# Kernel tuning notes

Measured on AMD Instinct MI355X. Metric: run time of the kernel, lower is better.

Reference implementation:

```python
import math
import jax, jax.numpy as jnp
import numpy as np

NUM_HEADS = 32

def _alibi_slopes(n: int) -> jnp.ndarray:
    cp2 = 2 ** int(math.floor(math.log2(n)))
    base = 2.0 ** (-(2.0 ** (-(math.log2(cp2) - 3))))
    slopes = base ** np.arange(1, cp2 + 1, dtype=np.float64)
    if cp2 != n:
        extra_base = 2.0 ** (-(2.0 ** (-(math.log2(2 * cp2) - 3))))
        rem = min(cp2, n - cp2)
        slopes = np.concatenate([slopes, extra_base ** np.arange(1, 1 + 2 * rem, 2, dtype=np.float64)])
    return jnp.asarray(slopes, dtype=jnp.float32)


def setup_inputs() -> dict:
    key = jax.random.key(0)
    k1, k2, k3 = jax.random.split(key, 3)
    B, S, E, H, D = 2, 2048, 4096, NUM_HEADS, 128
    hidden_states = jax.random.normal(k1, (B, S, E), dtype=jnp.float32)
    # torch Linear y = x @ W^T; we store transposed weights [in, out]
    w_qkv = jax.random.normal(k2, (E, H * D + 2 * D), dtype=jnp.float32) * 0.02
    w_c = jax.random.normal(k3, (E, E), dtype=jnp.float32) * 0.02
    return {"hidden_states": hidden_states, "w_qkv": w_qkv, "w_c": w_c}


def reference(hidden_states, w_qkv, w_c):
    B, S, E = hidden_states.shape
    H = NUM_HEADS
    D = E // H
    scaling = D ** -0.5

    qkv = hidden_states @ w_qkv                      # [B,S,H*D+2D]
    q = qkv[..., : H * D].reshape(B, S, H, D)        # [B,S,H,D]
    k = qkv[..., H * D: H * D + D]                   # [B,S,D] single KV head (MQA)
    v = qkv[..., H * D + D:]                         # [B,S,D]

    pos = jnp.arange(S)
    slopes = _alibi_slopes(H)                        # [H]
    # ALiBi: slope * (k_pos - q_pos), <= 0 in the causal region
    bias = slopes[:, None, None] * (pos[None, None, :] - pos[None, :, None]).astype(jnp.float32)  # [H,S,S]

    scores = jnp.einsum('bqhd,bkd->bhqk', q, k) * scaling + bias[None]  # [B,H,S,S]
    causal = pos[:, None] >= pos[None, :]            # [S,S]
    scores = jnp.where(causal[None, None], scores, jnp.finfo(scores.dtype).min)
    probs = jax.nn.softmax(scores, axis=-1)
    attn = jnp.einsum('bhqk,bkd->bqhd', probs, v).reshape(B, S, E)
    return attn @ w_c
```

## Files before the change

kernel.cpp:

```cpp
#include <hip/hip_runtime.h>
#include <hip/hip_bf16.h>

typedef unsigned short u16;
typedef unsigned int u32;
typedef __attribute__((ext_vector_type(8))) short s16x8;
typedef __attribute__((ext_vector_type(4))) float f32x4;

#define MFMA_BF16(a, b, c) __builtin_amdgcn_mfma_f32_16x16x32_bf16(a, b, c, 0, 0, 0)

__device__ __forceinline__ u16 f2bf(float f) {
  union { float f; u32 u; } c; c.f = f;
  return (u16)((c.u + 0x7FFFu + ((c.u >> 16) & 1u)) >> 16);
}

__device__ __forceinline__ u32 pkbf(float a, float b) {
  float2 t; t.x = a; t.y = b;
  __hip_bfloat162 h = __float22bfloat162_rn(t);
  union { __hip_bfloat162 h; u32 u; } c; c.h = h; return c.u;
}

__device__ __forceinline__ void gll16(const void* g, void* l) {
  __builtin_amdgcn_global_load_lds((const __attribute__((address_space(1))) void*)g,
                                   (__attribute__((address_space(3))) void*)l, 16, 0, 0);
}

__device__ __forceinline__ f32x4 f4zero() { f32x4 z = {0.f, 0.f, 0.f, 0.f}; return z; }

__global__ void cvt_bf16_kernel(const float4* __restrict__ in, u16* __restrict__ out, int n4) {
  int i = blockIdx.x * 256 + threadIdx.x;
  if (i >= n4) return;
  float4 v = in[i];
  uint2 w;
  w.x = (u32)f2bf(v.x) | ((u32)f2bf(v.y) << 16);
  w.y = (u32)f2bf(v.z) | ((u32)f2bf(v.w) << 16);
  *reinterpret_cast<uint2*>(out + (size_t)i * 4) = w;
}

__global__ void transpose_cvt_kernel(const float* __restrict__ in, u16* __restrict__ out,
                                     int R, int C) {
  __shared__ float tile[32][33];
  int tx = threadIdx.x, ty = threadIdx.y;
  int r0 = blockIdx.y * 32, c0 = blockIdx.x * 32;
#pragma unroll
  for (int i = 0; i < 32; i += 8)
    tile[ty + i][tx] = in[(size_t)(r0 + ty + i) * C + c0 + tx];
  __syncthreads();
#pragma unroll
  for (int i = 0; i < 32; i += 8)
    out[(size_t)(c0 + ty + i) * R + r0 + tx] = f2bf(tile[tx][ty + i]);
}


#define BARRIER __builtin_amdgcn_s_barrier()
#define LGKM0 asm volatile("s_waitcnt lgkmcnt(0)" ::: "memory")
#define PRIO1 __builtin_amdgcn_s_setprio(1)
#define PRIO0 __builtin_amdgcn_s_setprio(0)
#define VM6 asm volatile("s_waitcnt vmcnt(6)" ::: "memory")
#define VM4 asm volatile("s_waitcnt vmcnt(4)" ::: "memory")
#define VM2 asm volatile("s_waitcnt vmcnt(2)" ::: "memory")
#define VM0 asm volatile("s_waitcnt vmcnt(0)" ::: "memory")
#define NOPSTMT do {} while (0)
#define W1EPI do { if constexpr (EPI == 1) { VM6; } else { VM2; } } while (0)

#define RD_A(dst, PR, QM) do { _Pragma("unroll")                                         \
  for (int mi2 = 0; mi2 < 4; ++mi2) {                                                    \
    dst[mi2][0] = *(const s16x8*)(smem + (PR)*32768 + (QM)*16384 + mi2*2048 + aOff0);    \
    dst[mi2][1] = *(const s16x8*)(smem + (PR)*32768 + (QM)*16384 + mi2*2048 + aOff1);    \
  } } while (0)

#define RD_B(dst, PR, QN) do { _Pragma("unroll")                                         \
  for (int ni2 = 0; ni2 < 2; ++ni2) {                                                    \
    dst[ni2][0] = *(const s16x8*)(smem + 65536 + (PR)*32768 + (QN)*16384 + ni2*2048 + bOff0); \
    dst[ni2][1] = *(const s16x8*)(smem + 65536 + (PR)*32768 + (QN)*16384 + ni2*2048 + bOff1); \
  } } while (0)

#define MFMA_Q(QM, QN, Af, Bf) do { _Pragma("unroll")                                    \
  for (int ks = 0; ks < 2; ++ks) { _Pragma("unroll")                                     \
    for (int mi2 = 0; mi2 < 4; ++mi2) { _Pragma("unroll")                                \
      for (int ni2 = 0; ni2 < 2; ++ni2)                                                  \
        acc[(QM)*4+mi2][(QN)*2+ni2] =                                                    \
            MFMA_BF16(Af[mi2][ks], Bf[ni2][ks], acc[(QM)*4+mi2][(QN)*2+ni2]);            \
  } } } while (0)

#define STAGE_PAIR(x, PW, kn) do {                                                       \
  gll16(srcA[x] + (kn), smem + (PW)*32768 + (x)*8192 + tt*16);                           \
  gll16(srcB[x] + (kn), smem + 65536 + (PW)*32768 + (x)*8192 + tt*16);                   \
} while (0)

#define TILE_BODY(PR, KB, S1, S2, S3, S4, W1, W4) do {                                   \
  s16x8 a0[4][2], a1[4][2], b0[2][2], b1[2][2];                                          \
  s16x8 bkv[2][2]; s16x8 sa[2];                                                          \
                                                                           \
  RD_A(a0, PR, 0); RD_B(b0, PR, 0);                                                      \
  if constexpr (EPI == 1) {                                                              \
    const u16* kvp = Bt + (size_t)(4096 + w * 32 + li) * K + (KB) + g * 8;               \
    bkv[0][0] = *(const s16x8*)(kvp);                                                    \
    bkv[0][1] = *(const s16x8*)(kvp + 32);                                               \
    bkv[1][0] = *(const s16x8*)(kvp + (size_t)16 * K);                                   \
    bkv[1][1] = *(const s16x8*)(kvp + (size_t)16 * K + 32);                              \
  }                                                                                      \
  S1;                                                                                    \
  BARRIER; LGKM0; PRIO1; MFMA_Q(0, 0, a0, b0); PRIO0;                                    \
  W1; BARRIER;                                                                           \
                                                                           \
  RD_B(b1, PR, 1);                                                                       \
  S2;                                                                                    \
  BARRIER; LGKM0; PRIO1; MFMA_Q(0, 1, a0, b1); PRIO0; BARRIER;                           \
                                                                           \
  RD_A(a1, PR, 1);                                                                       \
  S3;                                                                                    \
  BARRIER; LGKM0; PRIO1; MFMA_Q(1, 1, a1, b1); PRIO0; BARRIER;                           \
                                                                \
  RD_B(b0, PR, 0);                                                                       \
  if constexpr (EPI == 1) {                                                              \
    sa[0] = *(const s16x8*)(smem + (PR)*32768 + aKV);                                    \
    sa[1] = *(const s16x8*)(smem + (PR)*32768 + (aKV ^ 64));                             \
  }                                                                                      \
  S4;                                                                                    \
  BARRIER; LGKM0; PRIO1; MFMA_Q(1, 0, a1, b0);                                           \
  if constexpr (EPI == 1) { _Pragma("unroll")                                            \
    for (int ks2 = 0; ks2 < 2; ++ks2) { _Pragma("unroll")                                \
      for (int cs2 = 0; cs2 < 2; ++cs2)                                                  \
        acc_kv[cs2] = MFMA_BF16(sa[ks2], bkv[cs2][ks2], acc_kv[cs2]);                    \
  } }                                                                                    \
  PRIO0; W4; BARRIER;                                                                    \
} while (0)

#define TILE_MAIN(PR, PW, T) TILE_BODY(PR, (T)*64,                                       \
  STAGE_PAIR(0, PW, ((T)+1)*64), STAGE_PAIR(1, PW, ((T)+1)*64),                          \
  STAGE_PAIR(2, PW, ((T)+1)*64), STAGE_PAIR(3, PW, ((T)+1)*64), W1EPI, VM4)
#define TILE_LAST(PR, T) TILE_BODY(PR, (T)*64, NOPSTMT, NOPSTMT, NOPSTMT, NOPSTMT, VM0, NOPSTMT)

template<int EPI>
__global__ __launch_bounds__(512, 2)
void gemm256_kernel(const u16* __restrict__ A, const u16* __restrict__ Bt,
                    float* __restrict__ Cf, u16* __restrict__ Cq,
                    u16* __restrict__ Ck, u16* __restrict__ Cvt,
                    int N, int K) {
  __shared__ __align__(16) char smem[131072];
  const int tt = threadIdx.x;
  const int w = tt >> 6, l = tt & 63;
  const int li = l & 15, g = l >> 4;
  const int wm = w >> 2, wn = w & 3;

  const int gx = gridDim.x;
  const int nwg = gx * gridDim.y;
  int id = blockIdx.y * gx + blockIdx.x;
  id = (id & 7) * (nwg >> 3) + (id >> 3);
  const int bn = id % gx, bm = id / gx;

  f32x4 acc[8][4];
#pragma unroll
  for (int i = 0; i < 8; ++i)
#pragma unroll
    for (int j = 0; j < 4; ++j) acc[i][j] = f4zero();
  f32x4 acc_kv[2];
  acc_kv[0] = f4zero(); acc_kv[1] = f4zero();

  const int q8 = (((tt & 7) ^ ((tt >> 3) & 7)) * 8);
  const u16* srcA[4];
  const u16* srcB[4];
#pragma unroll
  for (int x = 0; x < 4; ++x) {
    const int arow = (x & 1) * 128 + (x >> 1) * 64 + (tt >> 3);
    srcA[x] = A + (size_t)(bm * 256 + arow) * K + q8;
    const int rho = x * 64 + (tt >> 3);
    const int qn_ = rho >> 7, rem = rho & 127;
    const int wn_ = rem >> 5, rr = rem & 31;
    const int brow = wn_ * 64 + qn_ * 32 + rr;
    srcB[x] = Bt + (size_t)(bn * 256 + brow) * K + q8;
  }

  const int gr0 = (g ^ (li & 7)) * 16;
  const int aOff0 = wm * 8192 + li * 128 + gr0;
  const int aOff1 = aOff0 ^ 64;
  const int bOff0 = wn * 4096 + li * 128 + gr0;
  const int bOff1 = bOff0 ^ 64;
  const int aKV = ((bn >> 2) & 1) * 16384 + (bn >> 3) * 8192 + (bn & 3) * 2048
                  + li * 128 + gr0;

#pragma unroll
  for (int x = 0; x < 4; ++x) STAGE_PAIR(x, 0, 0);
  VM0;
  BARRIER;

  for (int t2 = 0; t2 < 62; t2 += 2) {
    TILE_MAIN(0, 1, t2);
    TILE_MAIN(1, 0, t2 + 1);
  }
  TILE_MAIN(0, 1, 62);
  TILE_LAST(1, 63);

#pragma unroll
  for (int mi = 0; mi < 8; ++mi) {
#pragma unroll
    for (int ni = 0; ni < 4; ++ni) {
      const int row0 = bm * 256 + wm * 128 + mi * 16 + g * 4;
      const int col = bn * 256 + wn * 64 + ni * 16 + li;
#pragma unroll
      for (int r = 0; r < 4; ++r) {
        const int m = row0 + r;
        const float v = acc[mi][ni][r];
        if (EPI == 0) {
          Cf[(size_t)m * N + col] = v;
        } else {
          Cq[(size_t)m * 4096 + col] = f2bf(v);
        }
      }
    }
  }
  if constexpr (EPI == 1) {
#pragma unroll
    for (int cs = 0; cs < 2; ++cs) {
      const int col = 4096 + w * 32 + cs * 16 + li;
#pragma unroll
      for (int r = 0; r < 4; ++r) {
        const int m = bm * 256 + bn * 16 + g * 4 + r;
        const float v = acc_kv[cs][r];
        const int bb2 = m >> 11, s = m & 2047;
        const int kt = s >> 5;
        const size_t tb = (size_t)(bb2 * 64 + kt);
        if (col < 4224) {
          const int d = col - 4096, kr = s & 31;
          const int mk = kr >> 4, lii = kr & 15;
          const int kk = d >> 5, gg = (d >> 3) & 3, e = d & 7;
          Ck[(tb * 8 + mk * 4 + kk) * 512 + (gg * 16 + lii) * 8 + e] = f2bf(v);
        } else {
          const int d = col - 4224, kp = s & 31;
          const int mf = d >> 4, lii = d & 15;
          const int gg = kp >> 3, e = kp & 7;
          Cvt[(tb * 8 + mf) * 512 + (gg * 16 + lii) * 8 + e] = f2bf(v);
        }
      }
    }
  }
}


__device__ __forceinline__ void load_ktile(s16x8 (&dst)[8], const u16* kf, size_t tb, int l) {
#pragma unroll
  for (int f = 0; f < 8; ++f)
    dst[f] = *(const s16x8*)&kf[(tb * 8 + f) * 512 + l * 8];
}

template<bool DIAG>
__device__ __forceinline__ void attn_tile(
    int kt, const u16* kf, const u16* vf, size_t bb64, int l, int li, int g,
    s16x8 (&use)[8], s16x8 (&fill)[8], bool do_fill,
    const s16x8 (&bq)[2][4], f32x4 (&acc)[8][2],
    float (&m_)[2], float (&lp)[2], float (&bias)[2],
    float c1, const float (&cjr)[8], float bstep, u16 (*Pw)[40]) {
  const size_t tb = bb64 + kt;
  s16x8 vr[8];
#pragma unroll
  for (int f = 0; f < 8; ++f)
    vr[f] = *(const s16x8*)&vf[(tb * 8 + f) * 512 + l * 8];
  if (do_fill) load_ktile(fill, kf, tb - 1, l);

  f32x4 sc[2][2];
  sc[0][0] = f4zero(); sc[0][1] = f4zero(); sc[1][0] = f4zero(); sc[1][1] = f4zero();
#pragma unroll
  for (int kk = 0; kk < 4; ++kk)
#pragma unroll
    for (int mk = 0; mk < 2; ++mk) {
      sc[mk][0] = MFMA_BF16(use[mk * 4 + kk], bq[0][kk], sc[mk][0]);
      sc[mk][1] = MFMA_BF16(use[mk * 4 + kk], bq[1][kk], sc[mk][1]);
    }

#pragma unroll
  for (int nq = 0; nq < 2; ++nq) {
    float sv[8];
    float pm = -3e38f;
    if (DIAG) {
#pragma unroll
      for (int mk = 0; mk < 2; ++mk)
#pragma unroll
        for (int r = 0; r < 4; ++r) {
          const int kd = mk * 16 + g * 4 + r - (nq * 16 + li);
          float s = fmaf(sc[mk][nq][r], c1, bias[nq] + cjr[mk * 4 + r]);
          s = (kd <= 0) ? s : -1e30f;
          sv[mk * 4 + r] = s;
          pm = fmaxf(pm, s);
        }
      pm = fmaxf(pm, __shfl_xor(pm, 16));
      pm = fmaxf(pm, __shfl_xor(pm, 32));
      m_[nq] = pm;
    } else {
#pragma unroll
      for (int mk = 0; mk < 2; ++mk)
#pragma unroll
        for (int r = 0; r < 4; ++r) {
          float s = fmaf(sc[mk][nq][r], c1, bias[nq] + cjr[mk * 4 + r]);
          sv[mk * 4 + r] = s;
          pm = fmaxf(pm, s);
        }
      if (__any(pm > m_[nq])) {
        pm = fmaxf(pm, __shfl_xor(pm, 16));
        pm = fmaxf(pm, __shfl_xor(pm, 32));
        const float nm = fmaxf(m_[nq], pm);
        const float scale = exp2f(m_[nq] - nm);
#pragma unroll
        for (int mf = 0; mf < 8; ++mf) acc[mf][nq] *= scale;
        lp[nq] *= scale;
        m_[nq] = nm;
      }
    }
    const float mref = m_[nq];
    float e[8];
#pragma unroll
    for (int j = 0; j < 8; ++j) e[j] = exp2f(sv[j] - mref);
    lp[nq] += ((e[0] + e[1]) + (e[2] + e[3])) + ((e[4] + e[5]) + (e[6] + e[7]));
#pragma unroll
    for (int mk = 0; mk < 2; ++mk) {
      uint2 wv;
      wv.x = pkbf(e[mk * 4 + 0], e[mk * 4 + 1]);
      wv.y = pkbf(e[mk * 4 + 2], e[mk * 4 + 3]);
      *reinterpret_cast<uint2*>(&Pw[nq * 16 + li][mk * 16 + g * 4]) = wv;
    }
    bias[nq] -= bstep;
  }

  s16x8 pb0 = *(const s16x8*)&Pw[li][g * 8];
  s16x8 pb1 = *(const s16x8*)&Pw[16 + li][g * 8];
#pragma unroll
  for (int mf = 0; mf < 8; ++mf) {
    acc[mf][0] = MFMA_BF16(vr[mf], pb0, acc[mf][0]);
    acc[mf][1] = MFMA_BF16(vr[mf], pb1, acc[mf][1]);
  }
}

__device__ __forceinline__ void attn_qtile(
    int qt, int h, int b, const u16* qbuf, const u16* kf, const u16* vf,
    u16* obuf, int l, int li, int g, float c1, float sl2, u16 (*Pw)[40]) {
  const int S = 2048;
  const int q0 = qt * 32;
  const size_t bb64 = (size_t)b * 64;

  s16x8 bq[2][4];
#pragma unroll
  for (int nq = 0; nq < 2; ++nq)
#pragma unroll
    for (int kk = 0; kk < 4; ++kk)
      bq[nq][kk] = *(const s16x8*)&qbuf[(size_t)(b * S + q0 + nq * 16 + li) * 4096
                                        + h * 128 + kk * 32 + g * 8];

  f32x4 acc[8][2];
#pragma unroll
  for (int mf = 0; mf < 8; ++mf) { acc[mf][0] = f4zero(); acc[mf][1] = f4zero(); }
  float m_[2] = {-3e38f, -3e38f};
  float lp[2] = {0.f, 0.f};

  float cjr[8];
#pragma unroll
  for (int j = 0; j < 8; ++j) cjr[j] = sl2 * (float)((j >> 2) * 16 + (j & 3));
  float bias[2];
#pragma unroll
  for (int nq = 0; nq < 2; ++nq)
    bias[nq] = sl2 * (float)(g * 4 - nq * 16 - li);
  const float bstep = sl2 * 32.f;

  s16x8 kA[8], kB[8];
  load_ktile(kA, kf, bb64 + qt, l);
  attn_tile<true>(qt, kf, vf, bb64, l, li, g, kA, kB, qt >= 1,
                  bq, acc, m_, lp, bias, c1, cjr, bstep, Pw);
  int kt = qt - 1;
  while (kt >= 1) {
    attn_tile<false>(kt, kf, vf, bb64, l, li, g, kB, kA, true,
                     bq, acc, m_, lp, bias, c1, cjr, bstep, Pw);
    attn_tile<false>(kt - 1, kf, vf, bb64, l, li, g, kA, kB, kt >= 2,
                     bq, acc, m_, lp, bias, c1, cjr, bstep, Pw);
    kt -= 2;
  }
  if (kt == 0)
    attn_tile<false>(0, kf, vf, bb64, l, li, g, kB, kA, false,
                     bq, acc, m_, lp, bias, c1, cjr, bstep, Pw);

#pragma unroll
  for (int nq = 0; nq < 2; ++nq) {
    float ls = lp[nq];
    ls += __shfl_xor(ls, 16);
    ls += __shfl_xor(ls, 32);
    const float inv = 1.f / ls;
    const size_t rowbase = (size_t)(b * S + q0 + nq * 16 + li) * 4096 + h * 128;
#pragma unroll
    for (int mf = 0; mf < 8; ++mf) {
      f32x4 v = acc[mf][nq];
      uint2 wv;
      wv.x = pkbf(v[0] * inv, v[1] * inv);
      wv.y = pkbf(v[2] * inv, v[3] * inv);
      *reinterpret_cast<uint2*>(&obuf[rowbase + mf * 16 + g * 4]) = wv;
    }
  }
}

__global__ __launch_bounds__(64, 2)
void attn_kernel(const u16* __restrict__ qbuf, const u16* __restrict__ kf,
                 const u16* __restrict__ vf, u16* __restrict__ obuf) {
  const int p = blockIdx.x, h = blockIdx.y, b = blockIdx.z;
  const int l = threadIdx.x, li = l & 15, g = l >> 4;
  const float L2E = 1.4426950408889634f;
  const float slope = exp2f(-0.25f * (float)(h + 1));
  const float c1 = 0.08838834764831845f * L2E;
  const float sl2 = slope * L2E;
  __shared__ __align__(16) u16 P[32][40];
  attn_qtile(63 - p, h, b, qbuf, kf, vf, obuf, l, li, g, c1, sl2, P);
  attn_qtile(p, h, b, qbuf, kf, vf, obuf, l, li, g, c1, sl2, P);
}

extern "C" void kernel_launch(void* const* d_in, const int* in_sizes, int n_in,
                              void* d_out, int out_size, void* d_ws, size_t ws_size,
                              hipStream_t stream) {
  (void)in_sizes; (void)n_in; (void)out_size; (void)ws_size;
  const float* hidden = (const float*)d_in[0];
  const float* w_qkv = (const float*)d_in[1];
  const float* w_c = (const float*)d_in[2];
  float* out = (float*)d_out;
  char* ws = (char*)d_ws;

  u16* hid_bf = (u16*)(ws + 0);
  u16* wT     = (u16*)(ws + 33554432);
  u16* qbuf   = (u16*)(ws + 69206016);
  u16* kbuf   = (u16*)(ws + 102760448);
  u16* vtbuf  = (u16*)(ws + 103809024);

  cvt_bf16_kernel<<<16384, 256, 0, stream>>>((const float4*)hidden, hid_bf, 4194304);
  transpose_cvt_kernel<<<dim3(136, 128), dim3(32, 8), 0, stream>>>(w_qkv, wT, 4096, 4352);
  gemm256_kernel<1><<<dim3(16, 16), 512, 0, stream>>>(hid_bf, wT, nullptr, qbuf, kbuf, vtbuf,
                                                      4352, 4096);
  attn_kernel<<<dim3(32, 32, 2), 64, 0, stream>>>(qbuf, kbuf, vtbuf, hid_bf);
  transpose_cvt_kernel<<<dim3(128, 128), dim3(32, 8), 0, stream>>>(w_c, wT, 4096, 4096);
  gemm256_kernel<0><<<dim3(16, 16), 512, 0, stream>>>(hid_bf, wT, out, nullptr, nullptr, nullptr,
                                                      4096, 4096);
}
```

Baseline: 485.8 us.

## Restructure GEMM main loop into two K-half phases with register double-buffered fragments

```diff
diff --git a/kernel.cpp b/kernel.cpp
--- a/kernel.cpp
+++ b/kernel.cpp
@@ -53,83 +53,73 @@
 
 #define BARRIER __builtin_amdgcn_s_barrier()
 #define LGKM0 asm volatile("s_waitcnt lgkmcnt(0)" ::: "memory")
+#define LGKM12 asm volatile("s_waitcnt lgkmcnt(12)" ::: "memory")
 #define PRIO1 __builtin_amdgcn_s_setprio(1)
 #define PRIO0 __builtin_amdgcn_s_setprio(0)
-#define VM6 asm volatile("s_waitcnt vmcnt(6)" ::: "memory")
-#define VM4 asm volatile("s_waitcnt vmcnt(4)" ::: "memory")
-#define VM2 asm volatile("s_waitcnt vmcnt(2)" ::: "memory")
 #define VM0 asm volatile("s_waitcnt vmcnt(0)" ::: "memory")
-#define NOPSTMT do {} while (0)
-#define W1EPI do { if constexpr (EPI == 1) { VM6; } else { VM2; } } while (0)
-
-#define RD_A(dst, PR, QM) do { _Pragma("unroll")                                         \
-  for (int mi2 = 0; mi2 < 4; ++mi2) {                                                    \
-    dst[mi2][0] = *(const s16x8*)(smem + (PR)*32768 + (QM)*16384 + mi2*2048 + aOff0);    \
-    dst[mi2][1] = *(const s16x8*)(smem + (PR)*32768 + (QM)*16384 + mi2*2048 + aOff1);    \
+
+#define RD12(AA, BB, PRB, KX) do { _Pragma("unroll")                                     \
+  for (int q = 0; q < 2; ++q) { _Pragma("unroll")                                        \
+    for (int m = 0; m < 4; ++m)                                                          \
+      AA[q*4+m] = *(const s16x8*)(smem + (PRB) + q*16384 + m*2048 + (aOff0 ^ (KX))); }   \
+  _Pragma("unroll")                                                                      \
+  for (int q = 0; q < 2; ++q) { _Pragma("unroll")                                        \
+    for (int n = 0; n < 2; ++n)                                                          \
+      BB[q*2+n] = *(const s16x8*)(smem + 65536 + (PRB) + q*16384 + n*2048 + (bOff0 ^ (KX))); } \
+} while (0)
+
+#define MFMA32(AA, BB) do { _Pragma("unroll")                                            \
+  for (int q = 0; q < 2; ++q) { _Pragma("unroll")                                        \
+    for (int m = 0; m < 4; ++m) { _Pragma("unroll")                                      \
+      for (int p = 0; p < 2; ++p) { _Pragma("unroll")                                    \
+        for (int n = 0; n < 2; ++n)                                                      \
+          acc[q*4+m][p*2+n] = MFMA_BF16(AA[q*4+m], BB[p*2+n], acc[q*4+m][p*2+n]);        \
+  } } } } while (0)
+
+#define STAGE4(PWB, kn) do { _Pragma("unroll")                                           \
+  for (int x = 0; x < 4; ++x) {                                                          \
+    gll16(srcA0 + (size_t)ADROW[x] * K + (kn), smem + (PWB) + x*8192 + tt*16);           \
+    gll16(srcB[x] + (kn), smem + 65536 + (PWB) + x*8192 + tt*16);                        \
   } } while (0)
 
-#define RD_B(dst, PR, QN) do { _Pragma("unroll")                                         \
-  for (int ni2 = 0; ni2 < 2; ++ni2) {                                                    \
-    dst[ni2][0] = *(const s16x8*)(smem + 65536 + (PR)*32768 + (QN)*16384 + ni2*2048 + bOff0); \
-    dst[ni2][1] = *(const s16x8*)(smem + 65536 + (PR)*32768 + (QN)*16384 + ni2*2048 + bOff1); \
-  } } while (0)
-
-#define MFMA_Q(QM, QN, Af, Bf) do { _Pragma("unroll")                                    \
-  for (int ks = 0; ks < 2; ++ks) { _Pragma("unroll")                                     \
-    for (int mi2 = 0; mi2 < 4; ++mi2) { _Pragma("unroll")                                \
-      for (int ni2 = 0; ni2 < 2; ++ni2)                                                  \
-        acc[(QM)*4+mi2][(QN)*2+ni2] =                                                    \
-            MFMA_BF16(Af[mi2][ks], Bf[ni2][ks], acc[(QM)*4+mi2][(QN)*2+ni2]);            \
-  } } } while (0)
-
-#define STAGE_PAIR(x, PW, kn) do {                                                       \
-  gll16(srcA[x] + (kn), smem + (PW)*32768 + (x)*8192 + tt*16);                           \
-  gll16(srcB[x] + (kn), smem + 65536 + (PW)*32768 + (x)*8192 + tt*16);                   \
+#define TILE(PRB, PWB, T, LAST) do {                                                     \
+               \
+  if constexpr (EPI == 1) {                                                              \
+    const u16* kvp = Bt + (size_t)(4096 + w * 32 + li) * K + (T) * 64 + g * 8;           \
+    bkv[0] = *(const s16x8*)(kvp);                                                       \
+    bkv[1] = *(const s16x8*)(kvp + (size_t)16 * K);                                      \
+    sa = *(const s16x8*)(smem + (PRB) + aKV);                                            \
+  }                                                                                      \
+  RD12(Ab, Bb, PRB, 64);                                                                 \
+  if (!(LAST)) { STAGE4(PWB, ((T) + 1) * 64); }                                          \
+  BARRIER;                                                                               \
+  LGKM12;                                                                                \
+  PRIO1; MFMA32(Aa, Ba);                                                                 \
+  if constexpr (EPI == 1) {                                                              \
+    acc_kv[0] = MFMA_BF16(sa, bkv[0], acc_kv[0]);                                        \
+    acc_kv[1] = MFMA_BF16(sa, bkv[1], acc_kv[1]);                                        \
+  }                                                                                      \
+  PRIO0;                                                                                 \
+  VM0;                                                                                   \
+  BARRIER;                                                                               \
+            \
+  if constexpr (EPI == 1) {                                                              \
+    const u16* kvp = Bt + (size_t)(4096 + w * 32 + li) * K + (T) * 64 + g * 8;           \
+    bkv[0] = *(const s16x8*)(kvp + 32);                                                  \
+    bkv[1] = *(const s16x8*)(kvp + (size_t)16 * K + 32);                                 \
+    sa = *(const s16x8*)(smem + (PRB) + (aKV ^ 64));                                     \
+  }                                                                                      \
+  if (!(LAST)) { RD12(Aa, Ba, PWB, 0); }                                                 \
+  BARRIER;                                                                               \
+  if (LAST) { LGKM0; } else { LGKM12; }                                                  \
+  PRIO1; MFMA32(Ab, Bb);                                                                 \
+  if constexpr (EPI == 1) {                                                              \
+    acc_kv[0] = MFMA_BF16(sa, bkv[0], acc_kv[0]);                                        \
+    acc_kv[1] = MFMA_BF16(sa, bkv[1], acc_kv[1]);                                        \
+  }                                                                                      \
+  PRIO0;                                                                                 \
+  BARRIER;                                                                               \
 } while (0)
-
-#define TILE_BODY(PR, KB, S1, S2, S3, S4, W1, W4) do {                                   \
-  s16x8 a0[4][2], a1[4][2], b0[2][2], b1[2][2];                                          \
-  s16x8 bkv[2][2]; s16x8 sa[2];                                                          \
-                                                                           \
-  RD_A(a0, PR, 0); RD_B(b0, PR, 0);                                                      \
-  if constexpr (EPI == 1) {                                                              \
-    const u16* kvp = Bt + (size_t)(4096 + w * 32 + li) * K + (KB) + g * 8;               \
-    bkv[0][0] = *(const s16x8*)(kvp);                                                    \
-    bkv[0][1] = *(const s16x8*)(kvp + 32);                                               \
-    bkv[1][0] = *(const s16x8*)(kvp + (size_t)16 * K);                                   \
-    bkv[1][1] = *(const s16x8*)(kvp + (size_t)16 * K + 32);                              \
-  }                                                                                      \
-  S1;                                                                                    \
-  BARRIER; LGKM0; PRIO1; MFMA_Q(0, 0, a0, b0); PRIO0;                                    \
-  W1; BARRIER;                                                                           \
-                                                                           \
-  RD_B(b1, PR, 1);                                                                       \
-  S2;                                                                                    \
-  BARRIER; LGKM0; PRIO1; MFMA_Q(0, 1, a0, b1); PRIO0; BARRIER;                           \
-                                                                           \
-  RD_A(a1, PR, 1);                                                                       \
-  S3;                                                                                    \
-  BARRIER; LGKM0; PRIO1; MFMA_Q(1, 1, a1, b1); PRIO0; BARRIER;                           \
-                                                                \
-  RD_B(b0, PR, 0);                                                                       \
-  if constexpr (EPI == 1) {                                                              \
-    sa[0] = *(const s16x8*)(smem + (PR)*32768 + aKV);                                    \
-    sa[1] = *(const s16x8*)(smem + (PR)*32768 + (aKV ^ 64));                             \
-  }                                                                                      \
-  S4;                                                                                    \
-  BARRIER; LGKM0; PRIO1; MFMA_Q(1, 0, a1, b0);                                           \
-  if constexpr (EPI == 1) { _Pragma("unroll")                                            \
-    for (int ks2 = 0; ks2 < 2; ++ks2) { _Pragma("unroll")                                \
-      for (int cs2 = 0; cs2 < 2; ++cs2)                                                  \
-        acc_kv[cs2] = MFMA_BF16(sa[ks2], bkv[cs2][ks2], acc_kv[cs2]);                    \
-  } }                                                                                    \
-  PRIO0; W4; BARRIER;                                                                    \
-} while (0)
-
-#define TILE_MAIN(PR, PW, T) TILE_BODY(PR, (T)*64,                                       \
-  STAGE_PAIR(0, PW, ((T)+1)*64), STAGE_PAIR(1, PW, ((T)+1)*64),                          \
-  STAGE_PAIR(2, PW, ((T)+1)*64), STAGE_PAIR(3, PW, ((T)+1)*64), W1EPI, VM4)
-#define TILE_LAST(PR, T) TILE_BODY(PR, (T)*64, NOPSTMT, NOPSTMT, NOPSTMT, NOPSTMT, VM0, NOPSTMT)
 
 template<int EPI>
 __global__ __launch_bounds__(512, 2)
@@ -142,6 +132,7 @@
   const int w = tt >> 6, l = tt & 63;
   const int li = l & 15, g = l >> 4;
   const int wm = w >> 2, wn = w & 3;
+  constexpr int ADROW[4] = {0, 128, 64, 192};
 
   const int gx = gridDim.x;
   const int nwg = gx * gridDim.y;
@@ -158,12 +149,10 @@
   acc_kv[0] = f4zero(); acc_kv[1] = f4zero();
 
   const int q8 = (((tt & 7) ^ ((tt >> 3) & 7)) * 8);
-  const u16* srcA[4];
+  const u16* srcA0 = A + (size_t)(bm * 256 + (tt >> 3)) * K + q8;
   const u16* srcB[4];
 #pragma unroll
   for (int x = 0; x < 4; ++x) {
-    const int arow = (x & 1) * 128 + (x >> 1) * 64 + (tt >> 3);
-    srcA[x] = A + (size_t)(bm * 256 + arow) * K + q8;
     const int rho = x * 64 + (tt >> 3);
     const int qn_ = rho >> 7, rem = rho & 127;
     const int wn_ = rem >> 5, rr = rem & 31;
@@ -173,23 +162,24 @@
 
   const int gr0 = (g ^ (li & 7)) * 16;
   const int aOff0 = wm * 8192 + li * 128 + gr0;
-  const int aOff1 = aOff0 ^ 64;
   const int bOff0 = wn * 4096 + li * 128 + gr0;
-  const int bOff1 = bOff0 ^ 64;
   const int aKV = ((bn >> 2) & 1) * 16384 + (bn >> 3) * 8192 + (bn & 3) * 2048
                   + li * 128 + gr0;
 
-#pragma unroll
-  for (int x = 0; x < 4; ++x) STAGE_PAIR(x, 0, 0);
+  s16x8 Aa[8], Ba[4], Ab[8], Bb[4];
+  s16x8 bkv[2], sa;
+
+  STAGE4(0, 0);
   VM0;
   BARRIER;
+  RD12(Aa, Ba, 0, 0);
 
   for (int t2 = 0; t2 < 62; t2 += 2) {
-    TILE_MAIN(0, 1, t2);
-    TILE_MAIN(1, 0, t2 + 1);
-  }
-  TILE_MAIN(0, 1, 62);
-  TILE_LAST(1, 63);
+    TILE(0, 32768, t2, 0);
+    TILE(32768, 0, t2 + 1, 0);
+  }
+  TILE(0, 32768, 62, 0);
+  TILE(32768, 0, 63, 1);
 
 #pragma unroll
   for (int mi = 0; mi < 8; ++mi) {
```

Measured after the change: 872.4 us. 1.8x slower.
